# Performance work log

Hardware: AMD Instinct MI355X
Metric: run time of the kernel (lower is better)

The kernel has to match this reference:

```python
import jax, jax.numpy as jnp
import numpy as np

B, N, SK, D, H = 4, 1024, 1024, 1024, 16
HD = D // H  # head_dim = 64


def _ln(x, w, b):
    # torch LayerNorm: biased variance, eps=1e-6
    m = x.mean(-1, keepdims=True)
    v = x.var(-1, keepdims=True)
    return (x - m) * jax.lax.rsqrt(v + 1e-6) * w + b


def setup_inputs() -> dict:
    key = jax.random.key(0)
    ks = jax.random.split(key, 16)
    def w(k, shape, s=0.02):
        return jax.random.normal(k, shape, jnp.float32) * s
    return dict(
        x=jax.random.normal(ks[0], (B, N, D), jnp.float32),
        k=jax.random.normal(ks[1], (N, H, SK, HD), jnp.float32),
        v=jax.random.normal(ks[2], (N, H, SK, HD), jnp.float32),
        qkv_w=w(ks[3], (D, 3 * D)), qkv_b=w(ks[4], (3 * D,)),
        sa_proj_w=w(ks[5], (D, D)), sa_proj_b=w(ks[6], (D,)),
        q_w=w(ks[7], (D, D)), q_b=w(ks[8], (D,)),
        ed_proj_w=w(ks[9], (D, D)), ed_proj_b=w(ks[10], (D,)),
        fc1_w=w(ks[11], (D, 4 * D)), fc1_b=w(ks[12], (4 * D,)),
        fc2_w=w(ks[13], (4 * D, D)), fc2_b=w(ks[14], (D,)),
        ln1_w=jnp.ones((D,)), ln1_b=jnp.zeros((D,)),
        ln2_w=jnp.ones((D,)), ln2_b=jnp.zeros((D,)),
        ln3_w=jnp.ones((D,)), ln3_b=jnp.zeros((D,)),
    )


def reference(x, k, v, qkv_w, qkv_b, sa_proj_w, sa_proj_b, q_w, q_b,
              ed_proj_w, ed_proj_b, fc1_w, fc1_b, fc2_w, fc2_b,
              ln1_w, ln1_b, ln2_w, ln2_b, ln3_w, ln3_b):
    scale = HD ** -0.5
    # ---- SelfAttention (faithful to the original, unusual einsums) ----
    qkv = (x @ qkv_w + qkv_b).reshape(B, N, 3, H, HD).transpose(2, 1, 3, 0, 4)
    q_s, k_s, v_s = qkv[0], qkv[1], qkv[2]  # each [N, H, B, HD]
    # no shared contraction index between k and q -> outer product of reductions
    dp = jnp.einsum('kabc,qdef->qabe', k_s, q_s) * scale  # [N, H, B, B]
    sc = jax.nn.softmax(dp, axis=-1)  # attn_p = 0.0 -> dropout is identity
    wa = jnp.einsum('qabc,kdef->bqaf', sc, v_s).reshape(B, N, D)
    sa = wa @ sa_proj_w + sa_proj_b
    h1 = _ln(sa + x, ln1_w, ln1_b)
    # ---- EncoderDecoderAttention ----
    qc = (h1 @ q_w + q_b).reshape(B, N, H, HD).transpose(1, 2, 0, 3)  # [N, H, B, HD]
    dp2 = jnp.einsum('abkd,abqd->abqk', k, qc) * scale  # [N, H, B, SK]
    sc2 = jax.nn.softmax(dp2, axis=-1)
    wa2 = jnp.einsum('abts,abse->tabe', sc2, v).reshape(B, N, D)
    ca = wa2 @ ed_proj_w + ed_proj_b
    h2 = _ln(ca + x, ln2_w, ln2_b)  # residual uses x (as in source)
    # ---- MLP (exact GELU, p=0 dropout) ----
    z = jax.nn.gelu(h2 @ fc1_w + fc1_b, approximate=False) @ fc2_w + fc2_b
    return _ln(z + h2, ln3_w, ln3_b)
```

## Files before the change

### kernel.cpp

```cpp
#include <hip/hip_runtime.h>
#include <hip/hip_bf16.h>
#include <math.h>

typedef __attribute__((ext_vector_type(8))) short bf16x8;
typedef __attribute__((ext_vector_type(4))) float f32x4;

__device__ __forceinline__ void gll16(const void* g, const void* l) {
  __builtin_amdgcn_global_load_lds((__attribute__((address_space(1))) void*)g,
                                   (__attribute__((address_space(3))) void*)l, 16, 0, 0);
}

__device__ __forceinline__ unsigned short bf16bits(float f) {
  __hip_bfloat16 h = __float2bfloat16(f);
  return *reinterpret_cast<unsigned short*>(&h);
}

__global__ __launch_bounds__(256) void k_transpose4(
    const float* __restrict__ W0, __hip_bfloat16* __restrict__ T0,
    const float* __restrict__ W1, __hip_bfloat16* __restrict__ T1,
    const float* __restrict__ W2, __hip_bfloat16* __restrict__ T2,
    const float* __restrict__ W3, __hip_bfloat16* __restrict__ T3)
{
  __shared__ float t[32][33];
  int b = blockIdx.x;
  const float* W; __hip_bfloat16* T; int R, C, bx, by;
  if (b < 1024)      { W = W0; T = T0; R = 1024; C = 1024; bx = b & 31;  by = b >> 5; }
  else if (b < 2048) { b -= 1024; W = W1; T = T1; R = 1024; C = 1024; bx = b & 31;  by = b >> 5; }
  else if (b < 6144) { b -= 2048; W = W2; T = T2; R = 1024; C = 4096; bx = b & 127; by = b >> 7; }
  else               { b -= 6144; W = W3; T = T3; R = 4096; C = 1024; bx = b & 31;  by = b >> 5; }
  const int c0 = bx << 5, r0 = by << 5;
  const int tx = threadIdx.x & 31, ty = threadIdx.x >> 5;
#pragma unroll
  for (int i = 0; i < 32; i += 8)
    t[ty + i][tx] = W[(size_t)(r0 + ty + i) * C + c0 + tx];
  __syncthreads();
#pragma unroll
  for (int i = 0; i < 32; i += 8)
    T[(size_t)(c0 + ty + i) * R + r0 + tx] = __float2bfloat16(t[tx][ty + i]);
}

__global__ __launch_bounds__(256) void k_colsum_part(const float* __restrict__ x, float* __restrict__ part) {
  const int d = blockIdx.x * 256 + threadIdx.x;
  const int r0 = blockIdx.y * 128;
  float acc = 0.f;
  for (int r = 0; r < 128; ++r) acc += x[(size_t)(r0 + r) * 1024 + d];
  part[blockIdx.y * 1024 + d] = acc;
}

__global__ __launch_bounds__(256) void k_matvec_t(const float* __restrict__ part,
                                                  const float* __restrict__ qkv_w,
                                                  float* __restrict__ tmpt) {
  __shared__ float xs[1024];
  __shared__ float red[8][32];
#pragma unroll
  for (int jj = 0; jj < 4; ++jj) {
    const int d = threadIdx.x + (jj << 8);
    float a = 0.f;
    for (int y = 0; y < 32; ++y) a += part[y * 1024 + d];
    xs[d] = a;
  }
  __syncthreads();
  const int j = blockIdx.x * 32 + (threadIdx.x & 31);
  const int rg = threadIdx.x >> 5;
  float acc = 0.f;
  for (int r = rg; r < 1024; r += 8)
    acc += xs[r] * qkv_w[(size_t)r * 3072 + 2048 + j];
  red[rg][threadIdx.x & 31] = acc;
  __syncthreads();
  if (threadIdx.x < 32) {
    float s = 0.f;
    for (int gq = 0; gq < 8; ++gq) s += red[gq][threadIdx.x];
    tmpt[blockIdx.x * 32 + threadIdx.x] = s;
  }
}

__global__ __launch_bounds__(256) void k_matvec_sa(const float* __restrict__ tmpt,
                                                   const float* __restrict__ qkv_b,
                                                   const float* __restrict__ saw,
                                                   const float* __restrict__ sab,
                                                   float* __restrict__ sarow) {
  __shared__ float vs[64];
  __shared__ float red[8][32];
  if (threadIdx.x < 64) {
    float a = 0.f;
    for (int h = 0; h < 16; ++h)
      a += tmpt[h * 64 + threadIdx.x] + 4096.0f * qkv_b[2048 + h * 64 + threadIdx.x];
    vs[threadIdx.x] = a;
  }
  __syncthreads();
  const int j = blockIdx.x * 32 + (threadIdx.x & 31);
  const int rg = threadIdx.x >> 5;
  float acc = 0.f;
  for (int r = rg; r < 1024; r += 8)
    acc += vs[r & 63] * saw[(size_t)r * 1024 + j];
  red[rg][threadIdx.x & 31] = acc;
  __syncthreads();
  if (threadIdx.x < 32) {
    float s = 0.f;
    for (int gq = 0; gq < 8; ++gq) s += red[gq][threadIdx.x];
    sarow[blockIdx.x * 32 + threadIdx.x] = s + sab[blockIdx.x * 32 + threadIdx.x];
  }
}

__global__ __launch_bounds__(256) void k_ln(
    const float* __restrict__ a, const float* __restrict__ b, const float* __restrict__ c,
    const float* __restrict__ rowadd, const float* __restrict__ w,
    const float* __restrict__ bias, float* __restrict__ outF,
    __hip_bfloat16* __restrict__ outB)
{
  const size_t base = (size_t)blockIdx.x * 1024;
  const int d4 = threadIdx.x << 2;
  float4 t = *(const float4*)(a + base + d4);
  if (b) { const float4 u = *(const float4*)(b + base + d4);
           t.x += u.x; t.y += u.y; t.z += u.z; t.w += u.w; }
  if (c) { const float4 u = *(const float4*)(c + base + d4);
           t.x += u.x; t.y += u.y; t.z += u.z; t.w += u.w; }
  if (rowadd) { const float4 u = *(const float4*)(rowadd + d4);
                t.x += u.x; t.y += u.y; t.z += u.z; t.w += u.w; }
  float s1 = t.x + t.y + t.z + t.w;
  float s2 = t.x * t.x + t.y * t.y + t.z * t.z + t.w * t.w;
#pragma unroll
  for (int o = 32; o; o >>= 1) { s1 += __shfl_xor(s1, o); s2 += __shfl_xor(s2, o); }
  __shared__ float r1[4], r2[4];
  const int wv = threadIdx.x >> 6;
  if ((threadIdx.x & 63) == 0) { r1[wv] = s1; r2[wv] = s2; }
  __syncthreads();
  s1 = r1[0] + r1[1] + r1[2] + r1[3];
  s2 = r2[0] + r2[1] + r2[2] + r2[3];
  const float mean = s1 * (1.0f / 1024.0f);
  const float var = s2 * (1.0f / 1024.0f) - mean * mean;
  const float inv = rsqrtf(var + 1e-6f);
  const float4 w4 = *(const float4*)(w + d4);
  const float4 b4 = *(const float4*)(bias + d4);
  const float y0 = (t.x - mean) * inv * w4.x + b4.x;
  const float y1 = (t.y - mean) * inv * w4.y + b4.y;
  const float y2 = (t.z - mean) * inv * w4.z + b4.z;
  const float y3 = (t.w - mean) * inv * w4.w + b4.w;
  if (outF) *(float4*)(outF + base + d4) = make_float4(y0, y1, y2, y3);
  if (outB) {
    ushort4 u4; u4.x = bf16bits(y0); u4.y = bf16bits(y1); u4.z = bf16bits(y2); u4.w = bf16bits(y3);
    *(ushort4*)(outB + base + d4) = u4;
  }
}

template<int GELU, int OUTBF>
__global__ __launch_bounds__(256) void k_gemm_bt(
    const __hip_bfloat16* __restrict__ A, const __hip_bfloat16* __restrict__ BT,
    const float* __restrict__ bias, float* __restrict__ outF, float* __restrict__ outF2,
    __hip_bfloat16* __restrict__ outB, int M, int N, int K)
{
  __shared__ __align__(16) __hip_bfloat16 As[128 * 32];
  __shared__ __align__(16) __hip_bfloat16 Bs[128 * 32];
  const int tid = threadIdx.x;
  const int wave = tid >> 6, lane = tid & 63;
  const int m0 = blockIdx.y << 7, n0 = blockIdx.x << 7;
  const int kl = K / gridDim.z;
  const int ks = blockIdx.z * kl;
  float* outP = blockIdx.z ? outF2 : outF;
  const bool doBias = (blockIdx.z == 0);
  const int wr = wave >> 1, wc = wave & 1;
  const int fr = lane & 15, fq = lane >> 4;
  f32x4 acc[4][4] = {};
  const int srow = (lane >> 2);
  const int scol = (lane & 3) * 8;
  for (int k0 = ks; k0 < ks + kl; k0 += 32) {
#pragma unroll
    for (int i = 0; i < 2; ++i) {
      const int chunk = wave * 2 + i;
      const int row = (chunk << 4) + srow;
      gll16(A + (size_t)(m0 + row) * K + k0 + scol, As + (chunk << 9));
      gll16(BT + (size_t)(n0 + row) * K + k0 + scol, Bs + (chunk << 9));
    }
    __syncthreads();
    bf16x8 af[4], bfr[4];
#pragma unroll
    for (int m = 0; m < 4; ++m)
      af[m] = *(const bf16x8*)(As + ((wr << 6) + (m << 4) + fr) * 32 + (fq << 3));
#pragma unroll
    for (int nn = 0; nn < 4; ++nn)
      bfr[nn] = *(const bf16x8*)(Bs + ((wc << 6) + (nn << 4) + fr) * 32 + (fq << 3));
#pragma unroll
    for (int m = 0; m < 4; ++m)
#pragma unroll
      for (int nn = 0; nn < 4; ++nn)
        acc[m][nn] = __builtin_amdgcn_mfma_f32_16x16x32_bf16(af[m], bfr[nn], acc[m][nn], 0, 0, 0);
    __syncthreads();
  }
#pragma unroll
  for (int m = 0; m < 4; ++m) {
#pragma unroll
    for (int nn = 0; nn < 4; ++nn) {
      const int col = n0 + (wc << 6) + (nn << 4) + fr;
      const float bv = doBias ? bias[col] : 0.f;
#pragma unroll
      for (int j = 0; j < 4; ++j) {
        const int row = m0 + (wr << 6) + (m << 4) + (fq << 2) + j;
        float vv = acc[m][nn][j] + bv;
        if (GELU) vv = 0.5f * vv * (1.0f + erff(vv * 0.70710678118654752f));
        if (OUTBF) outB[(size_t)row * N + col] = __float2bfloat16(vv);
        else       outP[(size_t)row * N + col] = vv;
      }
    }
  }
}

__global__ __launch_bounds__(256) void k_attn(
    const float* __restrict__ kk, const float* __restrict__ vvg,
    const float* __restrict__ qc1, const float* __restrict__ qc2,
    __hip_bfloat16* __restrict__ wa2b)
{
  __shared__ __align__(16) float tile[2][64 * 64];
  __shared__ __align__(16) float ql[4 * 64];
  const int tid = threadIdx.x;
  const int wave = tid >> 6, lane = tid & 63;
  const int n = blockIdx.x >> 4, h = blockIdx.x & 15;
  const size_t kvbase = (size_t)(n * 16 + h) * (1024 * 64);

  {
    const size_t qidx = ((size_t)wave * 1024 + n) * 1024 + h * 64 + lane;
    ql[tid] = (qc1[qidx] + qc2[qidx]) * 0.125f;
  }

  auto STAGE = [&](const float* __restrict__ src, int bi, int s0) {
#pragma unroll
    for (int i = 0; i < 4; ++i) {
      const int chunk = (wave << 2) + i;
      const int rl = (chunk << 2) + (lane >> 4);
      const int slot = (lane & 15) ^ (rl & 15);
      gll16(src + kvbase + (size_t)(s0 + rl) * 64 + (slot << 2), tile[bi] + (chunk << 8));
    }
  };

  STAGE(kk, 0, 0);
  __syncthreads();

  float preg[16];
  const int sx = lane & 15;
  const float* qrow = ql + wave * 64;
#pragma unroll
  for (int t = 0; t < 16; ++t) {
    if (t < 15) STAGE(kk, (t + 1) & 1, (t + 1) << 6);
    else        STAGE(vvg, 0, 0);
    const float* tl = tile[t & 1];
    float a0 = 0.f;
#pragma unroll
    for (int d4 = 0; d4 < 16; ++d4) {
      const float4 kv = *(const float4*)(tl + lane * 64 + ((d4 ^ sx) << 2));
      const float4 qa = *(const float4*)(qrow + (d4 << 2));
      a0 += kv.x * qa.x + kv.y * qa.y + kv.z * qa.z + kv.w * qa.w;
    }
    preg[t] = a0;
    __syncthreads();
  }

  float mx = preg[0];
#pragma unroll
  for (int t = 1; t < 16; ++t) mx = fmaxf(mx, preg[t]);
#pragma unroll
  for (int o = 32; o; o >>= 1) mx = fmaxf(mx, __shfl_xor(mx, o));
  float sum = 0.f;
#pragma unroll
  for (int t = 0; t < 16; ++t) { preg[t] = __expf(preg[t] - mx); sum += preg[t]; }
#pragma unroll
  for (int o = 32; o; o >>= 1) sum += __shfl_xor(sum, o);
  const float inv = 1.0f / sum;

  const int sg = lane >> 4, e4 = lane & 15;
  float4 acc4 = make_float4(0.f, 0.f, 0.f, 0.f);
#pragma unroll
  for (int t = 0; t < 16; ++t) {
    if (t < 15) STAGE(vvg, (t + 1) & 1, (t + 1) << 6);
    const float* tl = tile[t & 1];
#pragma unroll
    for (int so = 0; so < 16; ++so) {
      const int s = (so << 2) + sg;
      const float pw = __shfl(preg[t], s);
      const float4 vv = *(const float4*)(tl + s * 64 + ((e4 ^ (s & 15)) << 2));
      acc4.x += pw * vv.x; acc4.y += pw * vv.y; acc4.z += pw * vv.z; acc4.w += pw * vv.w;
    }
    __syncthreads();
  }
#pragma unroll
  for (int o = 16; o <= 32; o <<= 1) {
    acc4.x += __shfl_xor(acc4.x, o); acc4.y += __shfl_xor(acc4.y, o);
    acc4.z += __shfl_xor(acc4.z, o); acc4.w += __shfl_xor(acc4.w, o);
  }
  if (sg == 0) {
    ushort4 u4;
    u4.x = bf16bits(acc4.x * inv); u4.y = bf16bits(acc4.y * inv);
    u4.z = bf16bits(acc4.z * inv); u4.w = bf16bits(acc4.w * inv);
    *(ushort4*)(wa2b + ((size_t)wave * 1024 + n) * 1024 + h * 64 + (e4 << 2)) = u4;
  }
}

extern "C" void kernel_launch(void* const* d_in, const int* in_sizes, int n_in,
                              void* d_out, int out_size, void* d_ws, size_t ws_size,
                              hipStream_t stream)
{
  (void)in_sizes; (void)n_in; (void)out_size; (void)ws_size;
  const float* x     = (const float*)d_in[0];
  const float* kin   = (const float*)d_in[1];
  const float* vin   = (const float*)d_in[2];
  const float* qkv_w = (const float*)d_in[3];
  const float* qkv_b = (const float*)d_in[4];
  const float* sa_w  = (const float*)d_in[5];
  const float* sa_b  = (const float*)d_in[6];
  const float* q_w   = (const float*)d_in[7];
  const float* q_b   = (const float*)d_in[8];
  const float* ed_w  = (const float*)d_in[9];
  const float* ed_b  = (const float*)d_in[10];
  const float* fc1_w = (const float*)d_in[11];
  const float* fc1_b = (const float*)d_in[12];
  const float* fc2_w = (const float*)d_in[13];
  const float* fc2_b = (const float*)d_in[14];
  const float* ln1_w = (const float*)d_in[15];
  const float* ln1_b = (const float*)d_in[16];
  const float* ln2_w = (const float*)d_in[17];
  const float* ln2_b = (const float*)d_in[18];
  const float* ln3_w = (const float*)d_in[19];
  const float* ln3_b = (const float*)d_in[20];
  float* out = (float*)d_out;

  char* ws = (char*)d_ws;
  constexpr size_t MB = 1024ull * 1024ull;
  float* part  = (float*)(ws + 0);
  float* tmpt  = (float*)(ws + 192 * 1024);
  float* sarow = (float*)(ws + 256 * 1024);
  float* bufA  = (float*)(ws + 1 * MB);
  float* bufB  = (float*)(ws + 17 * MB);
  __hip_bfloat16* h1b  = (__hip_bfloat16*)(ws + 33 * MB);
  float*          h2   = (float*)(ws + 41 * MB);
  __hip_bfloat16* h2b  = (__hip_bfloat16*)(ws + 57 * MB);
  __hip_bfloat16* g    = (__hip_bfloat16*)(ws + 65 * MB);
  __hip_bfloat16* qwT  = (__hip_bfloat16*)(ws + 97 * MB);
  __hip_bfloat16* edwT = (__hip_bfloat16*)(ws + 99 * MB);
  __hip_bfloat16* f1wT = (__hip_bfloat16*)(ws + 101 * MB);
  __hip_bfloat16* f2wT = (__hip_bfloat16*)(ws + 109 * MB);
  __hip_bfloat16* wa2b = h1b;

  k_transpose4<<<dim3(10240), 256, 0, stream>>>(q_w, qwT, ed_w, edwT, fc1_w, f1wT, fc2_w, f2wT);
  k_colsum_part<<<dim3(4, 32), 256, 0, stream>>>(x, part);
  k_matvec_t<<<dim3(32), 256, 0, stream>>>(part, qkv_w, tmpt);
  k_matvec_sa<<<dim3(32), 256, 0, stream>>>(tmpt, qkv_b, sa_w, sa_b, sarow);
  k_ln<<<dim3(4096), 256, 0, stream>>>(x, nullptr, nullptr, sarow, ln1_w, ln1_b, nullptr, h1b);
  k_gemm_bt<0, 0><<<dim3(8, 32, 2), 256, 0, stream>>>(h1b, qwT, q_b, bufA, bufB, nullptr, 4096, 1024, 1024);
  k_attn<<<dim3(16384), 256, 0, stream>>>(kin, vin, bufA, bufB, wa2b);
  k_gemm_bt<0, 0><<<dim3(8, 32, 2), 256, 0, stream>>>(wa2b, edwT, ed_b, bufA, bufB, nullptr, 4096, 1024, 1024);
  k_ln<<<dim3(4096), 256, 0, stream>>>(bufA, bufB, x, nullptr, ln2_w, ln2_b, h2, h2b);
  k_gemm_bt<1, 1><<<dim3(32, 32), 256, 0, stream>>>(h2b, f1wT, fc1_b, nullptr, nullptr, g, 4096, 4096, 1024);
  k_gemm_bt<0, 0><<<dim3(8, 32, 2), 256, 0, stream>>>(g, f2wT, fc2_b, bufA, bufB, nullptr, 4096, 1024, 4096);
  k_ln<<<dim3(4096), 256, 0, stream>>>(bufA, bufB, h2, nullptr, ln3_w, ln3_b, out, nullptr);
}
```

Baseline: 1.896 ms.

## Replace LDS-staged K/V tiles with direct global loads in cross-attention

```diff
diff --git a/kernel.cpp b/kernel.cpp
--- a/kernel.cpp
+++ b/kernel.cpp
@@ -204,13 +204,13 @@
   }
 }
 
-__global__ __launch_bounds__(256) void k_attn(
+__global__ __launch_bounds__(256, 8) void k_attn(
     const float* __restrict__ kk, const float* __restrict__ vvg,
     const float* __restrict__ qc1, const float* __restrict__ qc2,
     __hip_bfloat16* __restrict__ wa2b)
 {
-  __shared__ __align__(16) float tile[2][64 * 64];
-  __shared__ __align__(16) float ql[4 * 64];
+  __shared__ float p[4 * 1024];
+  __shared__ float ql[4 * 64];
   const int tid = threadIdx.x;
   const int wave = tid >> 6, lane = tid & 63;
   const int n = blockIdx.x >> 4, h = blockIdx.x & 15;
@@ -220,65 +220,48 @@
     const size_t qidx = ((size_t)wave * 1024 + n) * 1024 + h * 64 + lane;
     ql[tid] = (qc1[qidx] + qc2[qidx]) * 0.125f;
   }
-
-  auto STAGE = [&](const float* __restrict__ src, int bi, int s0) {
-#pragma unroll
-    for (int i = 0; i < 4; ++i) {
-      const int chunk = (wave << 2) + i;
-      const int rl = (chunk << 2) + (lane >> 4);
-      const int slot = (lane & 15) ^ (rl & 15);
-      gll16(src + kvbase + (size_t)(s0 + rl) * 64 + (slot << 2), tile[bi] + (chunk << 8));
+  const float* qrow = ql + wave * 64;
+
+  for (int t = 0; t < 16; ++t) {
+    const float* krow = kk + kvbase + ((size_t)((t << 6) + lane) << 6);
+    float a = 0.f;
+#pragma unroll
+    for (int d4 = 0; d4 < 16; ++d4) {
+      const float4 kv = *(const float4*)(krow + (d4 << 2));
+      const float4 qa = *(const float4*)(qrow + (d4 << 2));
+      a += kv.x * qa.x + kv.y * qa.y + kv.z * qa.z + kv.w * qa.w;
     }
-  };
-
-  STAGE(kk, 0, 0);
-  __syncthreads();
-
-  float preg[16];
-  const int sx = lane & 15;
-  const float* qrow = ql + wave * 64;
-#pragma unroll
-  for (int t = 0; t < 16; ++t) {
-    if (t < 15) STAGE(kk, (t + 1) & 1, (t + 1) << 6);
-    else        STAGE(vvg, 0, 0);
-    const float* tl = tile[t & 1];
-    float a0 = 0.f;
-#pragma unroll
-    for (int d4 = 0; d4 < 16; ++d4) {
-      const float4 kv = *(const float4*)(tl + lane * 64 + ((d4 ^ sx) << 2));
-      const float4 qa = *(const float4*)(qrow + (d4 << 2));
-      a0 += kv.x * qa.x + kv.y * qa.y + kv.z * qa.z + kv.w * qa.w;
-    }
-    preg[t] = a0;
-    __syncthreads();
-  }
-
-  float mx = preg[0];
-#pragma unroll
-  for (int t = 1; t < 16; ++t) mx = fmaxf(mx, preg[t]);
+    p[(wave << 10) + (t << 6) + lane] = a;
+  }
+
+  float mx = -1e30f;
+#pragma unroll
+  for (int j = 0; j < 16; ++j) mx = fmaxf(mx, p[(wave << 10) + (j << 6) + lane]);
 #pragma unroll
   for (int o = 32; o; o >>= 1) mx = fmaxf(mx, __shfl_xor(mx, o));
   float sum = 0.f;
 #pragma unroll
-  for (int t = 0; t < 16; ++t) { preg[t] = __expf(preg[t] - mx); sum += preg[t]; }
+  for (int j = 0; j < 16; ++j) {
+    const float e = __expf(p[(wave << 10) + (j << 6) + lane] - mx);
+    p[(wave << 10) + (j << 6) + lane] = e;
+    sum += e;
+  }
 #pragma unroll
   for (int o = 32; o; o >>= 1) sum += __shfl_xor(sum, o);
   const float inv = 1.0f / sum;
 
   const int sg = lane >> 4, e4 = lane & 15;
   float4 acc4 = make_float4(0.f, 0.f, 0.f, 0.f);
-#pragma unroll
   for (int t = 0; t < 16; ++t) {
-    if (t < 15) STAGE(vvg, (t + 1) & 1, (t + 1) << 6);
-    const float* tl = tile[t & 1];
+    const float* vb = vvg + kvbase + ((size_t)t << 12);
+    const float* prow = p + (wave << 10) + (t << 6);
 #pragma unroll
     for (int so = 0; so < 16; ++so) {
       const int s = (so << 2) + sg;
-      const float pw = __shfl(preg[t], s);
-      const float4 vv = *(const float4*)(tl + s * 64 + ((e4 ^ (s & 15)) << 2));
+      const float pw = prow[s];
+      const float4 vv = *(const float4*)(vb + (s << 6) + (e4 << 2));
       acc4.x += pw * vv.x; acc4.y += pw * vv.y; acc4.z += pw * vv.z; acc4.w += pw * vv.w;
     }
-    __syncthreads();
   }
 #pragma unroll
   for (int o = 16; o <= 32; o <<= 1) {
```

Result: slower. 6.774 ms (+257.3%).
